# Performance work log

Measured on AMD Instinct MI355X. Metric: run time of the kernel, lower is better.

## Reference

```python
import jax, jax.numpy as jnp
import numpy as np

N_TOKENS = 16384
DIM = 2048
N_EXPERTS = 64
TOPK = 8
ROUTE_SCALE = 1.0


def setup_inputs() -> dict:
    key = jax.random.key(0)
    k1, k2 = jax.random.split(key)
    x = jax.random.normal(k1, (N_TOKENS, DIM), dtype=jnp.float32)
    W = jax.random.normal(k2, (N_EXPERTS, DIM), dtype=jnp.float32) * 0.02
    return {"x": x, "W": W}


def reference(x, W):
    # linear scores: [tokens, n_experts]
    logits = jnp.einsum('td,ed->te', x, W)
    # softmax in float32 (score_func == 'softmax'); bias is None since dim != 64
    scores = jax.nn.softmax(logits.astype(jnp.float32), axis=-1)
    # top-k expert selection, then gather original scores at selected indices
    _, indices = jax.lax.top_k(scores, TOPK)
    weights = jnp.take_along_axis(scores, indices, axis=-1)
    # softmax path: no renormalization, just route scaling
    weights = (weights * ROUTE_SCALE).astype(x.dtype)
    return weights, indices
```

## Files before the change

kernel.cpp:

```cpp
#include <hip/hip_runtime.h>


typedef __attribute__((ext_vector_type(8))) short short8;
typedef __attribute__((ext_vector_type(16))) float f32x16;
typedef __attribute__((ext_vector_type(4))) float f32x4;
typedef __attribute__((ext_vector_type(4))) unsigned int u32x4;

#define NT    16384
#define DIMK  2048
#define NE    64
#define TOPKK 8
#define TT    64
#define WS_BYTES (32 * 24 * 1024)

union U4S8 { unsigned int u[4]; short8 s; u32x4 v; };

__device__ __forceinline__ short8 as_s8(u32x4 v) { U4S8 t; t.v = v; return t.s; }

__device__ __forceinline__ void split3(const float4 a, const float4 b,
                                       short8& H, short8& M, short8& L) {
    const float f[8] = {a.x, a.y, a.z, a.w, b.x, b.y, b.z, b.w};
    U4S8 uh, um, ul;
#pragma unroll
    for (int p = 0; p < 4; ++p) {
        const float f0 = f[2 * p], f1 = f[2 * p + 1];
        const unsigned int t0 = __float_as_uint(f0) & 0xFFFF0000u;
        const unsigned int t1 = __float_as_uint(f1) & 0xFFFF0000u;
        uh.u[p] = (t0 >> 16) | t1;
        const float r0 = f0 - __uint_as_float(t0);
        const float r1 = f1 - __uint_as_float(t1);
        const unsigned int v0 = __float_as_uint(r0) & 0xFFFF0000u;
        const unsigned int v1 = __float_as_uint(r1) & 0xFFFF0000u;
        um.u[p] = (v0 >> 16) | v1;
        const float s0 = r0 - __uint_as_float(v0);
        const float s1 = r1 - __uint_as_float(v1);
        ul.u[p] = (__float_as_uint(s0) >> 16) | (__float_as_uint(s1) & 0xFFFF0000u);
    }
    H = uh.s; M = um.s; L = ul.s;
}

__device__ __forceinline__ f32x16 mfma6w(short8 ah, short8 am, short8 al,
                                         short8 bh, short8 bm, short8 bl,
                                         f32x16 c) {
    c = __builtin_amdgcn_mfma_f32_32x32x16_bf16(ah, bh, c, 0, 0, 0);
    c = __builtin_amdgcn_mfma_f32_32x32x16_bf16(ah, bm, c, 0, 0, 0);
    c = __builtin_amdgcn_mfma_f32_32x32x16_bf16(am, bh, c, 0, 0, 0);
    c = __builtin_amdgcn_mfma_f32_32x32x16_bf16(ah, bl, c, 0, 0, 0);
    c = __builtin_amdgcn_mfma_f32_32x32x16_bf16(am, bm, c, 0, 0, 0);
    c = __builtin_amdgcn_mfma_f32_32x32x16_bf16(al, bh, c, 0, 0, 0);
    return c;
}

__global__ __launch_bounds__(64) void pack_w_kernel(
    const float* __restrict__ W, short* __restrict__ wpk)
{
    const int b  = blockIdx.x;
    const int c  = b >> 3, fg = b & 7;
    const int s  = fg >> 1, n32 = fg & 1;
    const int l  = threadIdx.x;
    const float* g = W + (size_t)(32 * n32 + (l & 31)) * DIMK
                       + 64 * c + 16 * s + 8 * (l >> 5);
    const float4 lo = *(const float4*)g;
    const float4 hi = *(const float4*)(g + 4);
    short8 H, M, L;
    split3(lo, hi, H, M, L);
    const size_t base = ((size_t)(c * 8 + fg) * 3) * 512 + l * 8;
    *(short8*)(wpk + base)        = H;
    *(short8*)(wpk + base + 512)  = M;
    *(short8*)(wpk + base + 1024) = L;
}

#define WLOAD3(d0, d1, d2, p)                                                 \
    asm volatile("global_load_dwordx4 %0, %3, off\n\t"                        \
                 "global_load_dwordx4 %1, %3, off offset:1024\n\t"            \
                 "global_load_dwordx4 %2, %3, off offset:2048"                \
                 : "=&v"(d0), "=&v"(d1), "=&v"(d2) : "v"(p))
#define WAITN(n) do {                                                         \
    asm volatile("s_waitcnt vmcnt(" #n ")" ::: "memory");                     \
    __builtin_amdgcn_sched_barrier(0);                                        \
} while (0)

__device__ __forceinline__ void async16(void* lds, const void* gp) {
    __builtin_amdgcn_global_load_lds(
        (const __attribute__((address_space(1))) unsigned int*)gp,
        (__attribute__((address_space(3))) unsigned int*)lds, 16, 0, 0);
}

__global__ __launch_bounds__(512, 1) void gate_main_kernel(
    const float* __restrict__ x, const short* __restrict__ wpk,
    float* __restrict__ out)
{
    __shared__ __align__(16) char smem[8 * 3 * 4096];

    const int tid = threadIdx.x;
    const int w   = tid >> 6;
    const int l   = tid & 63;
    const int r31 = l & 31;
    const int l5  = l >> 5;
    const int tw  = w & 1;
    const int kq  = w >> 2 >= 0 ? (w >> 1) : 0;
    const int bt0 = blockIdx.x * TT;

    char* wbase = smem + w * 12288;
    const int swr = (r31 & 7) ^ (((r31 >> 3) & 3) << 1);

    const int srow = l >> 3;
    const int sg0  = (l & 7) ^ srow;
    const float* xrow0 = x + (size_t)(bt0 + 32 * tw + srow) * DIMK + kq * 512;

#define STAGE_CHUNK(k) do {                                                   \
    _Pragma("unroll")                                                         \
    for (int i = 0; i < 4; ++i) {                                             \
        const float* gsrc = xrow0 + (size_t)(8 * i) * DIMK + (k) * 32         \
                          + ((sg0 ^ (2 * i)) << 2);                           \
        async16(wbase + ((k) % 3) * 4096 + i * 1024, gsrc);                   \
    }                                                                         \
} while (0)

    const short* wq0 = wpk + (size_t)kq * 98304 + l * 8;
    const short* wq1 = wq0 + 1536;

    f32x16 acc0, acc1;
#pragma unroll
    for (int i = 0; i < 16; ++i) { acc0[i] = 0.f; acc1[i] = 0.f; }

    u32x4 w0v[4][3], w1v[4][3];

    STAGE_CHUNK(0);
    STAGE_CHUNK(1);
    STAGE_CHUNK(2);
    WLOAD3(w0v[0][0], w0v[0][1], w0v[0][2], wq0); wq0 += 3072;
    WLOAD3(w1v[0][0], w1v[0][1], w1v[0][2], wq1); wq1 += 3072;
    WLOAD3(w0v[1][0], w0v[1][1], w0v[1][2], wq0); wq0 += 3072;
    WLOAD3(w1v[1][0], w1v[1][1], w1v[1][2], wq1); wq1 += 3072;
    WLOAD3(w0v[2][0], w0v[2][1], w0v[2][2], wq0); wq0 += 3072;
    WLOAD3(w1v[2][0], w1v[2][1], w1v[2][2], wq1); wq1 += 3072;

#define SLICE(t) do {                                                         \
    if ((t) <= 28) {                                                          \
        WLOAD3(w0v[((t)+3)&3][0], w0v[((t)+3)&3][1], w0v[((t)+3)&3][2], wq0); \
        wq0 += 3072;                                                          \
        WLOAD3(w1v[((t)+3)&3][0], w1v[((t)+3)&3][1], w1v[((t)+3)&3][2], wq1); \
        wq1 += 3072;                                                          \
    }                                                                         \
    if ((t) <= 1)            WAITN(18);                                       \
    else if ((t) == 29)      WAITN(12);                                       \
    else if ((t) == 30)      WAITN(6);                                        \
    else if ((t) == 31)      WAITN(0);                                        \
    else if (((t) & 1) || (t) == 2 || (t) == 28) WAITN(22);                   \
    else                     WAITN(26);                                       \
    {                                                                         \
        const char* xb = wbase + (((t) >> 1) % 3) * 4096;                     \
        const float4 a0 = *(const float4*)(xb + r31 * 128 +                   \
            (((((t) & 1) * 4 + 2 * l5 + 0) ^ swr) << 4));                     \
        const float4 a1 = *(const float4*)(xb + r31 * 128 +                   \
            (((((t) & 1) * 4 + 2 * l5 + 1) ^ swr) << 4));                     \
        short8 H, M, L;                                                       \
        split3(a0, a1, H, M, L);                                              \
        acc0 = mfma6w(H, M, L, as_s8(w0v[(t)&3][0]), as_s8(w0v[(t)&3][1]),    \
                      as_s8(w0v[(t)&3][2]), acc0);                            \
        acc1 = mfma6w(H, M, L, as_s8(w1v[(t)&3][0]), as_s8(w1v[(t)&3][1]),    \
                      as_s8(w1v[(t)&3][2]), acc1);                            \
    }                                                                         \
    if (((t) & 1) && (t) <= 25) STAGE_CHUNK(((t) + 5) >> 1);                  \
} while (0)

    SLICE(0);  SLICE(1);  SLICE(2);  SLICE(3);
    SLICE(4);  SLICE(5);  SLICE(6);  SLICE(7);
    SLICE(8);  SLICE(9);  SLICE(10); SLICE(11);
    SLICE(12); SLICE(13); SLICE(14); SLICE(15);
    SLICE(16); SLICE(17); SLICE(18); SLICE(19);
    SLICE(20); SLICE(21); SLICE(22); SLICE(23);
    SLICE(24); SLICE(25); SLICE(26); SLICE(27);
    SLICE(28); SLICE(29); SLICE(30); SLICE(31);

    __syncthreads();

    float* lg = (float*)smem;
#pragma unroll
    for (int r = 0; r < 16; ++r) {
        const int rowc = (r & 3) + 8 * (r >> 2) + 4 * l5;
        const int trow = 32 * tw + rowc;
        lg[(kq * TT + trow) * (NE + 1) + r31]      = acc0[r];
        lg[(kq * TT + trow) * (NE + 1) + 32 + r31] = acc1[r];
    }
    __syncthreads();

#pragma unroll
    for (int rr = 0; rr < (TT * NE) / 512; ++rr) {
        const int idx = tid + rr * 512;
        const int t = idx >> 6, e = idx & 63;
        lg[t * (NE + 1) + e] =
            (lg[t * (NE + 1) + e] + lg[(TT + t) * (NE + 1) + e]) +
            (lg[(2 * TT + t) * (NE + 1) + e] + lg[(3 * TT + t) * (NE + 1) + e]);
    }
    __syncthreads();

    if (tid < TT) {
        const float* rowp = lg + tid * (NE + 1);
        float mx = -3.402823466e38f;
        for (int e = 0; e < NE; ++e) mx = fmaxf(mx, rowp[e]);
        float sden = 0.f;
        for (int e = 0; e < NE; ++e) sden += expf(rowp[e] - mx);

        float tv[TOPKK];
        int   ti[TOPKK];
#pragma unroll
        for (int i = 0; i < TOPKK; ++i) { tv[i] = -3.402823466e38f; ti[i] = 0; }
        for (int e = 0; e < NE; ++e) {
            const float v = rowp[e];
            if (v > tv[TOPKK - 1]) {
                tv[TOPKK - 1] = v; ti[TOPKK - 1] = e;
#pragma unroll
                for (int q = TOPKK - 1; q > 0; --q) {
                    if (tv[q] > tv[q - 1]) {
                        const float fv = tv[q]; tv[q] = tv[q - 1]; tv[q - 1] = fv;
                        const int   iv = ti[q]; ti[q] = ti[q - 1]; ti[q - 1] = iv;
                    }
                }
            }
        }
        float* ow = out + (size_t)(bt0 + tid) * TOPKK;
        float* oi = out + (size_t)NT * TOPKK + (size_t)(bt0 + tid) * TOPKK;
#pragma unroll
        for (int i = 0; i < TOPKK; ++i) {
            ow[i] = expf(tv[i] - mx) / sden;
            oi[i] = (float)ti[i];
        }
    }
#undef SLICE
#undef STAGE_CHUNK
}

__device__ __forceinline__ f32x4 mfma6s(short8 ah, short8 am, short8 al,
                                        short8 bh, short8 bm, short8 bl, f32x4 c) {
    c = __builtin_amdgcn_mfma_f32_16x16x32_bf16(ah, bh, c, 0, 0, 0);
    c = __builtin_amdgcn_mfma_f32_16x16x32_bf16(ah, bm, c, 0, 0, 0);
    c = __builtin_amdgcn_mfma_f32_16x16x32_bf16(am, bh, c, 0, 0, 0);
    c = __builtin_amdgcn_mfma_f32_16x16x32_bf16(ah, bl, c, 0, 0, 0);
    c = __builtin_amdgcn_mfma_f32_16x16x32_bf16(am, bm, c, 0, 0, 0);
    c = __builtin_amdgcn_mfma_f32_16x16x32_bf16(al, bh, c, 0, 0, 0);
    return c;
}

__device__ __forceinline__ void load_step(const float* xp0, const float* xp1,
                                          const float* wp, int koff,
                                          float4 xb[2][2], float4 wb[4][2]) {
#pragma unroll
    for (int h = 0; h < 2; ++h) {
        xb[0][h] = *(const float4*)(xp0 + koff + 4 * h);
        xb[1][h] = *(const float4*)(xp1 + koff + 4 * h);
    }
#pragma unroll
    for (int n = 0; n < 4; ++n)
#pragma unroll
        for (int h = 0; h < 2; ++h)
            wb[n][h] = *(const float4*)(wp + (size_t)n * 16 * DIMK + koff + 4 * h);
}

__device__ __forceinline__ void do_step(const float4 xc[2][2], const float4 wc[4][2],
                                        f32x4 acc[2][4]) {
    short8 ah[2], am[2], al[2];
#pragma unroll
    for (int m = 0; m < 2; ++m) split3(xc[m][0], xc[m][1], ah[m], am[m], al[m]);
#pragma unroll
    for (int n = 0; n < 4; ++n) {
        short8 bh, bm, bl;
        split3(wc[n][0], wc[n][1], bh, bm, bl);
#pragma unroll
        for (int m = 0; m < 2; ++m)
            acc[m][n] = mfma6s(ah[m], am[m], al[m], bh, bm, bl, acc[m][n]);
    }
}

__global__ __launch_bounds__(256, 2) void gate_fallback_kernel(
    const float* __restrict__ x, const float* __restrict__ W,
    float* __restrict__ out)
{
    __shared__ float lg[4][32][NE + 1];
    const int tid = threadIdx.x;
    const int w = tid >> 6, l = tid & 63;
    const int j = l & 15, g = l >> 4;
    const int bt0 = blockIdx.x * 32;
    const int kb = w * 512;
    const float* xp0 = x + (size_t)(bt0 + j) * DIMK + kb + 8 * g;
    const float* xp1 = xp0 + (size_t)16 * DIMK;
    const float* wpp = W + (size_t)j * DIMK + kb + 8 * g;
    f32x4 acc[2][4];
#pragma unroll
    for (int m = 0; m < 2; ++m)
#pragma unroll
        for (int n = 0; n < 4; ++n) acc[m][n] = (f32x4){0.f, 0.f, 0.f, 0.f};
    float4 xA[2][2], wA[4][2], xB[2][2], wB[4][2];
    load_step(xp0, xp1, wpp, 0, xA, wA);
#pragma unroll 1
    for (int s = 0; s < 16; s += 2) {
        load_step(xp0, xp1, wpp, 32 * (s + 1), xB, wB);
        do_step(xA, wA, acc);
        if (s + 2 < 16) load_step(xp0, xp1, wpp, 32 * (s + 2), xA, wA);
        do_step(xB, wB, acc);
    }
#pragma unroll
    for (int m = 0; m < 2; ++m)
#pragma unroll
        for (int n = 0; n < 4; ++n)
#pragma unroll
            for (int q = 0; q < 4; ++q)
                lg[w][16 * m + 4 * g + q][16 * n + j] = acc[m][n][q];
    __syncthreads();
#pragma unroll
    for (int r = 0; r < 8; ++r) {
        const int idx = tid + r * 256;
        const int t = idx >> 6, e = idx & 63;
        lg[0][t][e] += lg[1][t][e] + lg[2][t][e] + lg[3][t][e];
    }
    __syncthreads();
    if (tid < 32) {
        const float* rowp = &lg[0][tid][0];
        float mx = -3.402823466e38f;
        for (int e = 0; e < NE; ++e) mx = fmaxf(mx, rowp[e]);
        float sden = 0.f;
        for (int e = 0; e < NE; ++e) sden += expf(rowp[e] - mx);
        float tv[TOPKK]; int ti[TOPKK];
#pragma unroll
        for (int i = 0; i < TOPKK; ++i) { tv[i] = -3.402823466e38f; ti[i] = 0; }
        for (int e = 0; e < NE; ++e) {
            const float v = rowp[e];
            if (v > tv[TOPKK - 1]) {
                tv[TOPKK - 1] = v; ti[TOPKK - 1] = e;
#pragma unroll
                for (int q = TOPKK - 1; q > 0; --q)
                    if (tv[q] > tv[q - 1]) {
                        const float fv = tv[q]; tv[q] = tv[q - 1]; tv[q - 1] = fv;
                        const int iv = ti[q]; ti[q] = ti[q - 1]; ti[q - 1] = iv;
                    }
            }
        }
        float* ow = out + (size_t)(bt0 + tid) * TOPKK;
        float* oi = out + (size_t)NT * TOPKK + (size_t)(bt0 + tid) * TOPKK;
#pragma unroll
        for (int i = 0; i < TOPKK; ++i) {
            ow[i] = expf(tv[i] - mx) / sden;
            oi[i] = (float)ti[i];
        }
    }
}

extern "C" void kernel_launch(void* const* d_in, const int* in_sizes, int n_in,
                              void* d_out, int out_size, void* d_ws, size_t ws_size,
                              hipStream_t stream) {
    const float* x = (const float*)d_in[0];
    const float* W = (const float*)d_in[1];
    float* out = (float*)d_out;
    if (ws_size >= (size_t)WS_BYTES) {
        short* wpk = (short*)d_ws;
        hipLaunchKernelGGL(pack_w_kernel, dim3(256), dim3(64), 0, stream, W, wpk);
        hipLaunchKernelGGL(gate_main_kernel, dim3(NT / TT), dim3(512), 0, stream,
                           x, wpk, out);
    } else {
        hipLaunchKernelGGL(gate_fallback_kernel, dim3(NT / 32), dim3(256), 0, stream,
                           x, W, out);
    }
}
```

Baseline: 51.64 us.

## Split gate GEMM over K across blocks with partial-logit buffer and combine kernel

The main kernel now assigns each block one K quarter for 256 tokens, so every wave handles 32 tokens over a 512-wide K slice. Partial logits go to a workspace buffer, and a separate combine kernel sums them and runs softmax and top-k with one thread per token. It also adds periodic block barriers to keep waves in step while they share the packed-W stream, and switches x loads to non-temporal. The cost is an extra kernel launch and a global round trip of 16 MB of partial logits. The old fallback for small workspaces is removed, so nothing runs if the workspace is too small.

```diff
diff --git a/kernel.cpp b/kernel.cpp
--- a/kernel.cpp
+++ b/kernel.cpp
@@ -10,8 +10,9 @@
 #define DIMK  2048
 #define NE    64
 #define TOPKK 8
-#define TT    64
-#define WS_BYTES (32 * 24 * 1024)
+#define WPK_BYTES 786432
+#define PL_BYTES  (4 * NT * NE * 4)
+#define WS_NEED   (WPK_BYTES + PL_BYTES)
 
 union U4S8 { unsigned int u[4]; short8 s; u32x4 v; };
 
@@ -80,15 +81,15 @@
     __builtin_amdgcn_sched_barrier(0);                                        \
 } while (0)
 
-__device__ __forceinline__ void async16(void* lds, const void* gp) {
+__device__ __forceinline__ void async16nt(void* lds, const void* gp) {
     __builtin_amdgcn_global_load_lds(
         (const __attribute__((address_space(1))) unsigned int*)gp,
-        (__attribute__((address_space(3))) unsigned int*)lds, 16, 0, 0);
-}
-
-__global__ __launch_bounds__(512, 1) void gate_main_kernel(
+        (__attribute__((address_space(3))) unsigned int*)lds, 16, 0, 2 );
+}
+
+__global__ __launch_bounds__(512, 1) void gate_ksplit_kernel(
     const float* __restrict__ x, const short* __restrict__ wpk,
-    float* __restrict__ out)
+    float* __restrict__ pl)
 {
     __shared__ __align__(16) char smem[8 * 3 * 4096];
 
@@ -97,23 +98,23 @@
     const int l   = tid & 63;
     const int r31 = l & 31;
     const int l5  = l >> 5;
-    const int tw  = w & 1;
-    const int kq  = w >> 2 >= 0 ? (w >> 1) : 0;
-    const int bt0 = blockIdx.x * TT;
+    const int tg  = blockIdx.x >> 2;
+    const int kq  = blockIdx.x & 3;
+    const int bt0 = tg * 256;
+    const int tokbase = bt0 + 32 * w;
 
     char* wbase = smem + w * 12288;
     const int swr = (r31 & 7) ^ (((r31 >> 3) & 3) << 1);
-
     const int srow = l >> 3;
     const int sg0  = (l & 7) ^ srow;
-    const float* xrow0 = x + (size_t)(bt0 + 32 * tw + srow) * DIMK + kq * 512;
+    const float* xrow0 = x + (size_t)(tokbase + srow) * DIMK + kq * 512;
 
 #define STAGE_CHUNK(k) do {                                                   \
     _Pragma("unroll")                                                         \
     for (int i = 0; i < 4; ++i) {                                             \
         const float* gsrc = xrow0 + (size_t)(8 * i) * DIMK + (k) * 32         \
                           + ((sg0 ^ (2 * i)) << 2);                           \
-        async16(wbase + ((k) % 3) * 4096 + i * 1024, gsrc);                   \
+        async16nt(wbase + ((k) % 3) * 4096 + i * 1024, gsrc);                 \
     }                                                                         \
 } while (0)
 
@@ -165,6 +166,163 @@
     if (((t) & 1) && (t) <= 25) STAGE_CHUNK(((t) + 5) >> 1);                  \
 } while (0)
 
+#define PBAR() __builtin_amdgcn_s_barrier()
+
+    SLICE(0);  SLICE(1);  SLICE(2);  SLICE(3);  PBAR();
+    SLICE(4);  SLICE(5);  SLICE(6);  SLICE(7);  PBAR();
+    SLICE(8);  SLICE(9);  SLICE(10); SLICE(11); PBAR();
+    SLICE(12); SLICE(13); SLICE(14); SLICE(15); PBAR();
+    SLICE(16); SLICE(17); SLICE(18); SLICE(19); PBAR();
+    SLICE(20); SLICE(21); SLICE(22); SLICE(23); PBAR();
+    SLICE(24); SLICE(25); SLICE(26); SLICE(27); PBAR();
+    SLICE(28); SLICE(29); SLICE(30); SLICE(31);
+
+    float* base0 = pl + ((size_t)kq * NT + tokbase) * NE;
+#pragma unroll
+    for (int r = 0; r < 16; ++r) {
+        const int rowc = (r & 3) + 8 * (r >> 2) + 4 * l5;
+        base0[rowc * NE + r31]      = acc0[r];
+        base0[rowc * NE + 32 + r31] = acc1[r];
+    }
+#undef SLICE
+#undef STAGE_CHUNK
+#undef PBAR
+}
+
+__global__ __launch_bounds__(64) void gate_combine_kernel(
+    const float* __restrict__ pl, float* __restrict__ out)
+{
+    const int g = blockIdx.x * 64 + threadIdx.x;
+    const f32x4* p0 = (const f32x4*)(pl + (size_t)g * NE);
+    const f32x4* p1 = (const f32x4*)(pl + ((size_t)NT + g) * NE);
+    const f32x4* p2 = (const f32x4*)(pl + ((size_t)2 * NT + g) * NE);
+    const f32x4* p3 = (const f32x4*)(pl + ((size_t)3 * NT + g) * NE);
+
+    f32x4 row[16];
+#pragma unroll
+    for (int j = 0; j < 16; ++j)
+        row[j] = (p0[j] + p1[j]) + (p2[j] + p3[j]);
+
+    float mx = -3.402823466e38f;
+#pragma unroll
+    for (int j = 0; j < 16; ++j)
+#pragma unroll
+        for (int c = 0; c < 4; ++c) mx = fmaxf(mx, row[j][c]);
+
+    float sden = 0.f;
+#pragma unroll
+    for (int j = 0; j < 16; ++j)
+#pragma unroll
+        for (int c = 0; c < 4; ++c) sden += expf(row[j][c] - mx);
+
+    float tv[TOPKK];
+    int   ti[TOPKK];
+#pragma unroll
+    for (int i = 0; i < TOPKK; ++i) { tv[i] = -3.402823466e38f; ti[i] = 0; }
+#pragma unroll
+    for (int j = 0; j < 16; ++j)
+#pragma unroll
+        for (int c = 0; c < 4; ++c) {
+            const float v = row[j][c];
+            const int   e = 4 * j + c;
+            if (v > tv[TOPKK - 1]) {
+                tv[TOPKK - 1] = v; ti[TOPKK - 1] = e;
+#pragma unroll
+                for (int q = TOPKK - 1; q > 0; --q) {
+                    if (tv[q] > tv[q - 1]) {
+                        const float fv = tv[q]; tv[q] = tv[q - 1]; tv[q - 1] = fv;
+                        const int   iv = ti[q]; ti[q] = ti[q - 1]; ti[q - 1] = iv;
+                    }
+                }
+            }
+        }
+
+    float* ow = out + (size_t)g * TOPKK;
+    float* oi = out + (size_t)NT * TOPKK + (size_t)g * TOPKK;
+#pragma unroll
+    for (int i = 0; i < TOPKK; ++i) {
+        ow[i] = expf(tv[i] - mx) / sden;
+        oi[i] = (float)ti[i];
+    }
+}
+
+__device__ __forceinline__ void async16(void* lds, const void* gp) {
+    __builtin_amdgcn_global_load_lds(
+        (const __attribute__((address_space(1))) unsigned int*)gp,
+        (__attribute__((address_space(3))) unsigned int*)lds, 16, 0, 0);
+}
+
+__global__ __launch_bounds__(512, 1) void gate_main_r8(
+    const float* __restrict__ x, const short* __restrict__ wpk,
+    float* __restrict__ out)
+{
+    __shared__ __align__(16) char smem[8 * 3 * 4096];
+    const int tid = threadIdx.x;
+    const int w   = tid >> 6;
+    const int l   = tid & 63;
+    const int r31 = l & 31;
+    const int l5  = l >> 5;
+    const int tw  = w & 1;
+    const int kq  = w >> 1;
+    const int bt0 = blockIdx.x * 64;
+    char* wbase = smem + w * 12288;
+    const int swr = (r31 & 7) ^ (((r31 >> 3) & 3) << 1);
+    const int srow = l >> 3;
+    const int sg0  = (l & 7) ^ srow;
+    const float* xrow0 = x + (size_t)(bt0 + 32 * tw + srow) * DIMK + kq * 512;
+
+#define STAGE_CHUNK(k) do {                                                   \
+    _Pragma("unroll")                                                         \
+    for (int i = 0; i < 4; ++i) {                                             \
+        const float* gsrc = xrow0 + (size_t)(8 * i) * DIMK + (k) * 32         \
+                          + ((sg0 ^ (2 * i)) << 2);                           \
+        async16(wbase + ((k) % 3) * 4096 + i * 1024, gsrc);                   \
+    }                                                                         \
+} while (0)
+
+    const short* wq0 = wpk + (size_t)kq * 98304 + l * 8;
+    const short* wq1 = wq0 + 1536;
+    f32x16 acc0, acc1;
+#pragma unroll
+    for (int i = 0; i < 16; ++i) { acc0[i] = 0.f; acc1[i] = 0.f; }
+    u32x4 w0v[4][3], w1v[4][3];
+    STAGE_CHUNK(0); STAGE_CHUNK(1); STAGE_CHUNK(2);
+    WLOAD3(w0v[0][0], w0v[0][1], w0v[0][2], wq0); wq0 += 3072;
+    WLOAD3(w1v[0][0], w1v[0][1], w1v[0][2], wq1); wq1 += 3072;
+    WLOAD3(w0v[1][0], w0v[1][1], w0v[1][2], wq0); wq0 += 3072;
+    WLOAD3(w1v[1][0], w1v[1][1], w1v[1][2], wq1); wq1 += 3072;
+    WLOAD3(w0v[2][0], w0v[2][1], w0v[2][2], wq0); wq0 += 3072;
+    WLOAD3(w1v[2][0], w1v[2][1], w1v[2][2], wq1); wq1 += 3072;
+
+#define SLICE(t) do {                                                         \
+    if ((t) <= 28) {                                                          \
+        WLOAD3(w0v[((t)+3)&3][0], w0v[((t)+3)&3][1], w0v[((t)+3)&3][2], wq0); \
+        wq0 += 3072;                                                          \
+        WLOAD3(w1v[((t)+3)&3][0], w1v[((t)+3)&3][1], w1v[((t)+3)&3][2], wq1); \
+        wq1 += 3072;                                                          \
+    }                                                                         \
+    if ((t) <= 1)            WAITN(18);                                       \
+    else if ((t) == 29)      WAITN(12);                                       \
+    else if ((t) == 30)      WAITN(6);                                        \
+    else if ((t) == 31)      WAITN(0);                                        \
+    else if (((t) & 1) || (t) == 2 || (t) == 28) WAITN(22);                   \
+    else                     WAITN(26);                                       \
+    {                                                                         \
+        const char* xb = wbase + (((t) >> 1) % 3) * 4096;                     \
+        const float4 a0 = *(const float4*)(xb + r31 * 128 +                   \
+            (((((t) & 1) * 4 + 2 * l5 + 0) ^ swr) << 4));                     \
+        const float4 a1 = *(const float4*)(xb + r31 * 128 +                   \
+            (((((t) & 1) * 4 + 2 * l5 + 1) ^ swr) << 4));                     \
+        short8 H, M, L;                                                       \
+        split3(a0, a1, H, M, L);                                              \
+        acc0 = mfma6w(H, M, L, as_s8(w0v[(t)&3][0]), as_s8(w0v[(t)&3][1]),    \
+                      as_s8(w0v[(t)&3][2]), acc0);                            \
+        acc1 = mfma6w(H, M, L, as_s8(w1v[(t)&3][0]), as_s8(w1v[(t)&3][1]),    \
+                      as_s8(w1v[(t)&3][2]), acc1);                            \
+    }                                                                         \
+    if (((t) & 1) && (t) <= 25) STAGE_CHUNK(((t) + 5) >> 1);                  \
+} while (0)
+
     SLICE(0);  SLICE(1);  SLICE(2);  SLICE(3);
     SLICE(4);  SLICE(5);  SLICE(6);  SLICE(7);
     SLICE(8);  SLICE(9);  SLICE(10); SLICE(11);
@@ -175,36 +333,31 @@
     SLICE(28); SLICE(29); SLICE(30); SLICE(31);
 
     __syncthreads();
-
     float* lg = (float*)smem;
 #pragma unroll
     for (int r = 0; r < 16; ++r) {
         const int rowc = (r & 3) + 8 * (r >> 2) + 4 * l5;
         const int trow = 32 * tw + rowc;
-        lg[(kq * TT + trow) * (NE + 1) + r31]      = acc0[r];
-        lg[(kq * TT + trow) * (NE + 1) + 32 + r31] = acc1[r];
+        lg[(kq * 64 + trow) * (NE + 1) + r31]      = acc0[r];
+        lg[(kq * 64 + trow) * (NE + 1) + 32 + r31] = acc1[r];
     }
     __syncthreads();
-
-#pragma unroll
-    for (int rr = 0; rr < (TT * NE) / 512; ++rr) {
+#pragma unroll
+    for (int rr = 0; rr < 8; ++rr) {
         const int idx = tid + rr * 512;
         const int t = idx >> 6, e = idx & 63;
         lg[t * (NE + 1) + e] =
-            (lg[t * (NE + 1) + e] + lg[(TT + t) * (NE + 1) + e]) +
-            (lg[(2 * TT + t) * (NE + 1) + e] + lg[(3 * TT + t) * (NE + 1) + e]);
+            (lg[t * (NE + 1) + e] + lg[(64 + t) * (NE + 1) + e]) +
+            (lg[(128 + t) * (NE + 1) + e] + lg[(192 + t) * (NE + 1) + e]);
     }
     __syncthreads();
-
-    if (tid < TT) {
+    if (tid < 64) {
         const float* rowp = lg + tid * (NE + 1);
         float mx = -3.402823466e38f;
         for (int e = 0; e < NE; ++e) mx = fmaxf(mx, rowp[e]);
         float sden = 0.f;
         for (int e = 0; e < NE; ++e) sden += expf(rowp[e] - mx);
-
-        float tv[TOPKK];
-        int   ti[TOPKK];
+        float tv[TOPKK]; int ti[TOPKK];
 #pragma unroll
         for (int i = 0; i < TOPKK; ++i) { tv[i] = -3.402823466e38f; ti[i] = 0; }
         for (int e = 0; e < NE; ++e) {
@@ -232,133 +385,23 @@
 #undef STAGE_CHUNK
 }
 
-__device__ __forceinline__ f32x4 mfma6s(short8 ah, short8 am, short8 al,
-                                        short8 bh, short8 bm, short8 bl, f32x4 c) {
-    c = __builtin_amdgcn_mfma_f32_16x16x32_bf16(ah, bh, c, 0, 0, 0);
-    c = __builtin_amdgcn_mfma_f32_16x16x32_bf16(ah, bm, c, 0, 0, 0);
-    c = __builtin_amdgcn_mfma_f32_16x16x32_bf16(am, bh, c, 0, 0, 0);
-    c = __builtin_amdgcn_mfma_f32_16x16x32_bf16(ah, bl, c, 0, 0, 0);
-    c = __builtin_amdgcn_mfma_f32_16x16x32_bf16(am, bm, c, 0, 0, 0);
-    c = __builtin_amdgcn_mfma_f32_16x16x32_bf16(al, bh, c, 0, 0, 0);
-    return c;
-}
-
-__device__ __forceinline__ void load_step(const float* xp0, const float* xp1,
-                                          const float* wp, int koff,
-                                          float4 xb[2][2], float4 wb[4][2]) {
-#pragma unroll
-    for (int h = 0; h < 2; ++h) {
-        xb[0][h] = *(const float4*)(xp0 + koff + 4 * h);
-        xb[1][h] = *(const float4*)(xp1 + koff + 4 * h);
-    }
-#pragma unroll
-    for (int n = 0; n < 4; ++n)
-#pragma unroll
-        for (int h = 0; h < 2; ++h)
-            wb[n][h] = *(const float4*)(wp + (size_t)n * 16 * DIMK + koff + 4 * h);
-}
-
-__device__ __forceinline__ void do_step(const float4 xc[2][2], const float4 wc[4][2],
-                                        f32x4 acc[2][4]) {
-    short8 ah[2], am[2], al[2];
-#pragma unroll
-    for (int m = 0; m < 2; ++m) split3(xc[m][0], xc[m][1], ah[m], am[m], al[m]);
-#pragma unroll
-    for (int n = 0; n < 4; ++n) {
-        short8 bh, bm, bl;
-        split3(wc[n][0], wc[n][1], bh, bm, bl);
-#pragma unroll
-        for (int m = 0; m < 2; ++m)
-            acc[m][n] = mfma6s(ah[m], am[m], al[m], bh, bm, bl, acc[m][n]);
-    }
-}
-
-__global__ __launch_bounds__(256, 2) void gate_fallback_kernel(
-    const float* __restrict__ x, const float* __restrict__ W,
-    float* __restrict__ out)
-{
-    __shared__ float lg[4][32][NE + 1];
-    const int tid = threadIdx.x;
-    const int w = tid >> 6, l = tid & 63;
-    const int j = l & 15, g = l >> 4;
-    const int bt0 = blockIdx.x * 32;
-    const int kb = w * 512;
-    const float* xp0 = x + (size_t)(bt0 + j) * DIMK + kb + 8 * g;
-    const float* xp1 = xp0 + (size_t)16 * DIMK;
-    const float* wpp = W + (size_t)j * DIMK + kb + 8 * g;
-    f32x4 acc[2][4];
-#pragma unroll
-    for (int m = 0; m < 2; ++m)
-#pragma unroll
-        for (int n = 0; n < 4; ++n) acc[m][n] = (f32x4){0.f, 0.f, 0.f, 0.f};
-    float4 xA[2][2], wA[4][2], xB[2][2], wB[4][2];
-    load_step(xp0, xp1, wpp, 0, xA, wA);
-#pragma unroll 1
-    for (int s = 0; s < 16; s += 2) {
-        load_step(xp0, xp1, wpp, 32 * (s + 1), xB, wB);
-        do_step(xA, wA, acc);
-        if (s + 2 < 16) load_step(xp0, xp1, wpp, 32 * (s + 2), xA, wA);
-        do_step(xB, wB, acc);
-    }
-#pragma unroll
-    for (int m = 0; m < 2; ++m)
-#pragma unroll
-        for (int n = 0; n < 4; ++n)
-#pragma unroll
-            for (int q = 0; q < 4; ++q)
-                lg[w][16 * m + 4 * g + q][16 * n + j] = acc[m][n][q];
-    __syncthreads();
-#pragma unroll
-    for (int r = 0; r < 8; ++r) {
-        const int idx = tid + r * 256;
-        const int t = idx >> 6, e = idx & 63;
-        lg[0][t][e] += lg[1][t][e] + lg[2][t][e] + lg[3][t][e];
-    }
-    __syncthreads();
-    if (tid < 32) {
-        const float* rowp = &lg[0][tid][0];
-        float mx = -3.402823466e38f;
-        for (int e = 0; e < NE; ++e) mx = fmaxf(mx, rowp[e]);
-        float sden = 0.f;
-        for (int e = 0; e < NE; ++e) sden += expf(rowp[e] - mx);
-        float tv[TOPKK]; int ti[TOPKK];
-#pragma unroll
-        for (int i = 0; i < TOPKK; ++i) { tv[i] = -3.402823466e38f; ti[i] = 0; }
-        for (int e = 0; e < NE; ++e) {
-            const float v = rowp[e];
-            if (v > tv[TOPKK - 1]) {
-                tv[TOPKK - 1] = v; ti[TOPKK - 1] = e;
-#pragma unroll
-                for (int q = TOPKK - 1; q > 0; --q)
-                    if (tv[q] > tv[q - 1]) {
-                        const float fv = tv[q]; tv[q] = tv[q - 1]; tv[q - 1] = fv;
-                        const int iv = ti[q]; ti[q] = ti[q - 1]; ti[q - 1] = iv;
-                    }
-            }
-        }
-        float* ow = out + (size_t)(bt0 + tid) * TOPKK;
-        float* oi = out + (size_t)NT * TOPKK + (size_t)(bt0 + tid) * TOPKK;
-#pragma unroll
-        for (int i = 0; i < TOPKK; ++i) {
-            ow[i] = expf(tv[i] - mx) / sden;
-            oi[i] = (float)ti[i];
-        }
-    }
-}
-
 extern "C" void kernel_launch(void* const* d_in, const int* in_sizes, int n_in,
                               void* d_out, int out_size, void* d_ws, size_t ws_size,
                               hipStream_t stream) {
     const float* x = (const float*)d_in[0];
     const float* W = (const float*)d_in[1];
     float* out = (float*)d_out;
-    if (ws_size >= (size_t)WS_BYTES) {
-        short* wpk = (short*)d_ws;
+    short* wpk = (short*)d_ws;
+    if (ws_size >= (size_t)WS_NEED) {
+        float* pl = (float*)((char*)d_ws + WPK_BYTES);
         hipLaunchKernelGGL(pack_w_kernel, dim3(256), dim3(64), 0, stream, W, wpk);
-        hipLaunchKernelGGL(gate_main_kernel, dim3(NT / TT), dim3(512), 0, stream,
+        hipLaunchKernelGGL(gate_ksplit_kernel, dim3(256), dim3(512), 0, stream,
+                           x, wpk, pl);
+        hipLaunchKernelGGL(gate_combine_kernel, dim3(NT / 64), dim3(64), 0, stream,
+                           pl, out);
+    } else if (ws_size >= (size_t)WPK_BYTES) {
+        hipLaunchKernelGGL(pack_w_kernel, dim3(256), dim3(64), 0, stream, W, wpk);
+        hipLaunchKernelGGL(gate_main_r8, dim3(NT / 64), dim3(512), 0, stream,
                            x, wpk, out);
-    } else {
-        hipLaunchKernelGGL(gate_fallback_kernel, dim3(NT / 32), dim3(256), 0, stream,
-                           x, W, out);
-    }
-}
+    }
+}
```

Result: slower. 61.63 us (+19.4%).
